# Kernel optimization log

Measured on AMD Instinct MI355X. Metric: run time of the kernel, lower is better.

Reference implementation:

```python
import jax, jax.numpy as jnp
import numpy as np

N_HEAD = 16

def setup_inputs() -> dict:
    key = jax.random.key(0)
    k1, k2, k3, k4, k5 = jax.random.split(key, 5)
    B, S, D = 2, 2048, 1024
    return {
        "hidden_states": jax.random.normal(k1, (B, S, D), jnp.float32),
        "w_attn": jax.random.normal(k2, (D, 3 * D), jnp.float32) * 0.02,
        "b_attn": jax.random.normal(k3, (3 * D,), jnp.float32) * 0.02,
        "w_proj": jax.random.normal(k4, (D, D), jnp.float32) * 0.02,
        "b_proj": jax.random.normal(k5, (D,), jnp.float32) * 0.02,
    }

def reference(hidden_states, w_attn, b_attn, w_proj, b_proj):
    B, S, D = hidden_states.shape
    H = N_HEAD
    Dh = D // H
    qkv = hidden_states @ w_attn + b_attn              # [B,S,3D]
    q, k, v = jnp.split(qkv, 3, axis=-1)
    def split_heads(x):
        return x.reshape(B, S, H, Dh).transpose(0, 2, 1, 3)  # [B,H,S,Dh]
    q, k, v = split_heads(q), split_heads(k), split_heads(v)
    # scale=True: divide by sqrt(head_dim) (v.size(-1))
    scores = jnp.einsum("bhqd,bhkd->bhqk", q, k) / jnp.sqrt(jnp.float32(Dh))
    attn = jax.nn.softmax(scores, axis=-1)             # [B,H,S,S]
    out = jnp.einsum("bhqk,bhkd->bhqd", attn, v)       # [B,H,S,Dh]
    out = out.transpose(0, 2, 1, 3).reshape(B, S, D)   # merge heads
    return out @ w_proj + b_proj
```

## Files before the change

kernel.cpp:

```cpp
#include <hip/hip_runtime.h>
#include <hip/hip_bf16.h>

typedef __attribute__((ext_vector_type(8))) short bf16x8;
typedef __attribute__((ext_vector_type(4))) float f32x4;
typedef __attribute__((ext_vector_type(16))) float f32x16;

#define LOG2E 1.4426950408889634f
#define SCALE_F (0.125f * LOG2E)

__device__ inline unsigned short f2bf(float f) {
  union { float f; unsigned u; } x; x.f = f;
  unsigned u = x.u;
  unsigned r = u + 0x7FFFu + ((u >> 16) & 1u);
  return (unsigned short)(r >> 16);
}

__device__ inline unsigned cvtpk(float lo, float hi) {
  unsigned r;
  asm("v_cvt_pk_bf16_f32 %0, %1, %2" : "=v"(r) : "v"(lo), "v"(hi));
  return r;
}

__device__ inline void gload16(const unsigned short* g, unsigned short* l) {
  __builtin_amdgcn_global_load_lds(
      (const __attribute__((address_space(1))) unsigned int*)g,
      (__attribute__((address_space(3))) unsigned int*)l, 16, 0, 0);
}

template <int J>
__device__ inline bf16x8 pack_pfrag(f32x16 p) {
  int X, Y, Z, W;
  asm("v_cvt_pk_bf16_f32 %0, %1, %2" : "=v"(X) : "v"(p[J + 0]), "v"(p[J + 1]));
  asm("v_cvt_pk_bf16_f32 %0, %1, %2" : "=v"(Y) : "v"(p[J + 2]), "v"(p[J + 3]));
  asm("v_cvt_pk_bf16_f32 %0, %1, %2" : "=v"(Z) : "v"(p[J + 4]), "v"(p[J + 5]));
  asm("v_cvt_pk_bf16_f32 %0, %1, %2" : "=v"(W) : "v"(p[J + 6]), "v"(p[J + 7]));
  asm("v_permlane32_swap_b32 %0, %1" : "+v"(X), "+v"(Z));
  asm("v_permlane32_swap_b32 %0, %1" : "+v"(Y), "+v"(W));
  union { int w[4]; bf16x8 v; } u;
  u.w[0] = X; u.w[1] = Y; u.w[2] = Z; u.w[3] = W;
  return u.v;
}

__device__ inline void transpose_tile(const float* __restrict__ W,
                                      unsigned short* __restrict__ WT, int K, int N,
                                      int n0, int k0, int t,
                                      unsigned short (*Tl)[72]) {
#pragma unroll
  for (int i = 0; i < 4; ++i) {
    int idx = t + i * 256;
    int r = idx >> 4, c4 = (idx & 15) << 2;
    float4 v = *reinterpret_cast<const float4*>(&W[(size_t)(k0 + r) * N + n0 + c4]);
    Tl[c4 + 0][r] = f2bf(v.x);
    Tl[c4 + 1][r] = f2bf(v.y);
    Tl[c4 + 2][r] = f2bf(v.z);
    Tl[c4 + 3][r] = f2bf(v.w);
  }
  __syncthreads();
#pragma unroll
  for (int i = 0; i < 2; ++i) {
    int idx = t + i * 256;
    int rr = idx >> 3, cc = (idx & 7) << 3;
    *reinterpret_cast<int4*>(&WT[(size_t)(n0 + rr) * K + k0 + cc]) =
        *reinterpret_cast<const int4*>(&Tl[rr][cc]);
  }
}

__global__ __launch_bounds__(256) void prep_fused(
    const float* __restrict__ hs, unsigned short* __restrict__ hs_b,
    const float* __restrict__ w_attn, unsigned short* __restrict__ wT,
    const float* __restrict__ w_proj, unsigned short* __restrict__ pT) {
  __shared__ unsigned short Tl[64][72];
  const int bid = blockIdx.x, t = threadIdx.x;
  if (bid < 768) {
    transpose_tile(w_attn, wT, 1024, 3072, (bid % 48) * 64, (bid / 48) * 64, t, Tl);
  } else if (bid < 1024) {
    int r = bid - 768;
    transpose_tile(w_proj, pT, 1024, 1024, (r % 16) * 64, (r / 16) * 64, t, Tl);
  } else {
    int cb = bid - 1024;
#pragma unroll
    for (int j = 0; j < 4; ++j) {
      int i = cb * 1024 + j * 256 + t;
      float4 v = reinterpret_cast<const float4*>(hs)[i];
      ushort4 o;
      o.x = f2bf(v.x); o.y = f2bf(v.y); o.z = f2bf(v.z); o.w = f2bf(v.w);
      reinterpret_cast<ushort4*>(hs_b)[i] = o;
    }
  }
}

__global__ __launch_bounds__(512, 2) void gemm_qkv_8p(
    const unsigned short* __restrict__ A, const unsigned short* __restrict__ Bt,
    const float* __restrict__ bias,
    unsigned short* __restrict__ qw, unsigned short* __restrict__ kw,
    unsigned short* __restrict__ vtg) {
  __shared__ unsigned short Abuf[2][16384];
  __shared__ unsigned short Bbuf[2][12288];
  const int t = threadIdx.x, lane = t & 63, wid = t >> 6;
  const int wm = wid >> 2, wn = wid & 3;
  const int orig = blockIdx.x;
  const int nid = (orig & 7) * 32 + (orig >> 3);
  const int mt = nid >> 4, nt = nid & 15;
  const int row0 = mt * 256, col0 = nt * 192;
  const int lr = lane & 15, kq = lane >> 4;
  const int srow_lo = lane >> 3;
  const int scg = (lane & 7) ^ srow_lo;
  const unsigned short* Ab = A + (size_t)row0 * 1024;
  const unsigned short* Bb = Bt + (size_t)col0 * 1024;
  f32x4 acc[8][3] = {};

#define SA8(bs, kt)                                                              \
  {                                                                              \
    const unsigned short* Ap = Ab + (kt) * 64;                                   \
    _Pragma("unroll") for (int i = 0; i < 4; ++i) {                              \
      int g = wid * 4 + i;                                                       \
      int rrel = g * 8 + srow_lo;                                                \
      gload16(&Ap[(size_t)rrel * 1024 + scg * 8], &Abuf[bs][g * 512]);           \
    }                                                                            \
  }
#define SB8(bs, kt)                                                              \
  {                                                                              \
    const unsigned short* Bp = Bb + (kt) * 64;                                   \
    _Pragma("unroll") for (int i = 0; i < 3; ++i) {                              \
      int g = wid * 3 + i;                                                       \
      int rrel = g * 8 + srow_lo;                                                \
      gload16(&Bp[(size_t)rrel * 1024 + scg * 8], &Bbuf[bs][g * 512]);           \
    }                                                                            \
  }
#define RDA(dst, mh)                                                             \
  _Pragma("unroll") for (int m = 0; m < 4; ++m)                                  \
  _Pragma("unroll") for (int ks = 0; ks < 2; ++ks) {                             \
    int row = wm * 128 + (mh) * 64 + m * 16 + lr;                                \
    dst[m][ks] = *reinterpret_cast<const bf16x8*>(                               \
        &Ac[row * 64 + (((ks * 4 + kq) ^ (row & 7)) << 3)]);                     \
  }
#define RDB2(dst)                                                                \
  _Pragma("unroll") for (int n = 0; n < 2; ++n)                                  \
  _Pragma("unroll") for (int ks = 0; ks < 2; ++ks) {                             \
    int row = wn * 48 + n * 16 + lr;                                             \
    dst[n][ks] = *reinterpret_cast<const bf16x8*>(                               \
        &Bc[row * 64 + (((ks * 4 + kq) ^ (row & 7)) << 3)]);                     \
  }
#define RDB1(dst)                                                                \
  _Pragma("unroll") for (int ks = 0; ks < 2; ++ks) {                             \
    int row = wn * 48 + 32 + lr;                                                 \
    dst[0][ks] = *reinterpret_cast<const bf16x8*>(                               \
        &Bc[row * 64 + (((ks * 4 + kq) ^ (row & 7)) << 3)]);                     \
  }
#define QMM2(mh, afv, bfv)                                                       \
  _Pragma("unroll") for (int m = 0; m < 4; ++m)                                  \
  _Pragma("unroll") for (int n = 0; n < 2; ++n)                                  \
  _Pragma("unroll") for (int ks = 0; ks < 2; ++ks)                               \
    acc[(mh) * 4 + m][n] = __builtin_amdgcn_mfma_f32_16x16x32_bf16(              \
        afv[m][ks], bfv[n][ks], acc[(mh) * 4 + m][n], 0, 0, 0);
#define QMM1(mh, afv, bfv)                                                       \
  _Pragma("unroll") for (int m = 0; m < 4; ++m)                                  \
  _Pragma("unroll") for (int ks = 0; ks < 2; ++ks)                               \
    acc[(mh) * 4 + m][2] = __builtin_amdgcn_mfma_f32_16x16x32_bf16(              \
        afv[m][ks], bfv[0][ks], acc[(mh) * 4 + m][2], 0, 0, 0);
#define BAR8 __builtin_amdgcn_s_barrier();

  SA8(0, 0) SB8(0, 0)
  asm volatile("s_waitcnt vmcnt(0)" ::: "memory");
  BAR8
  __builtin_amdgcn_sched_barrier(0);

  for (int kt = 0; kt < 16; ++kt) {
    const int buf = kt & 1;
    const unsigned short* Ac = Abuf[buf];
    const unsigned short* Bc = Bbuf[buf];
    bf16x8 af0[4][2], af1[4][2], bf0[2][2], bf1[1][2];
    RDA(af0, 0) RDB2(bf0)
    if (kt < 15) SA8(buf ^ 1, kt + 1)
    BAR8
    __builtin_amdgcn_s_setprio(1); QMM2(0, af0, bf0) __builtin_amdgcn_s_setprio(0);
    BAR8
    RDA(af1, 1)
    if (kt < 15) SB8(buf ^ 1, kt + 1)
    BAR8
    __builtin_amdgcn_s_setprio(1); QMM2(1, af1, bf0) __builtin_amdgcn_s_setprio(0);
    BAR8
    RDB1(bf1)
    BAR8
    __builtin_amdgcn_s_setprio(1); QMM1(0, af0, bf1) __builtin_amdgcn_s_setprio(0);
    BAR8
    if (kt < 15) { asm volatile("s_waitcnt vmcnt(0)" ::: "memory"); }
    BAR8
    __builtin_amdgcn_s_setprio(1); QMM1(1, af1, bf1) __builtin_amdgcn_s_setprio(0);
    BAR8
    __builtin_amdgcn_sched_barrier(0);
  }
#undef SA8
#undef SB8
#undef RDA
#undef RDB2
#undef RDB1
#undef QMM2
#undef QMM1
#undef BAR8

  const int rbase = (lane >> 4) * 4;
#pragma unroll
  for (int mm = 0; mm < 8; ++mm) {
#pragma unroll
    for (int nn = 0; nn < 3; ++nn) {
      int c = col0 + wn * 48 + nn * 16 + lr;
      int which = c >> 10;
      int d = c & 1023;
      int h = d >> 6, dh = d & 63;
      float bv = bias[c];
      int m0 = row0 + wm * 128 + mm * 16 + rbase;
      int b = m0 >> 11, s0 = m0 & 2047;
      if (which == 2) {
        int kt = s0 >> 6, key0 = s0 & 63;
        ushort4 pv;
        pv.x = f2bf(acc[mm][nn][0] + bv);
        pv.y = f2bf(acc[mm][nn][1] + bv);
        pv.z = f2bf(acc[mm][nn][2] + bv);
        pv.w = f2bf(acc[mm][nn][3] + bv);
        *reinterpret_cast<ushort4*>(
            &vtg[(((size_t)(b * 16 + h) * 32 + kt) * 64 + dh) * 64 + key0]) = pv;
      } else if (which == 1) {
#pragma unroll
        for (int r = 0; r < 4; ++r)
          kw[(((size_t)b * 16 + h) * 2048 + (s0 + r)) * 64 + dh] = f2bf(acc[mm][nn][r] + bv);
      } else {
#pragma unroll
        for (int r = 0; r < 4; ++r)
          qw[(((size_t)b * 16 + h) * 2048 + (s0 + r)) * 64 + dh] =
              f2bf((acc[mm][nn][r] + bv) * SCALE_F);
      }
    }
  }
}

#define GST(bs, kt)                                                             \
  {                                                                             \
    const unsigned short* Ap = Ab + (kt) * 32;                                  \
    const unsigned short* Bp = Bb + (kt) * 32;                                  \
    _Pragma("unroll") for (int i = 0; i < 2; ++i) {                             \
      int row = i * 64 + wid * 16 + s_r;                                        \
      gload16(&Ap[(size_t)row * 1024 + s_c], &Al[bs][i * 2048 + wid * 512]);    \
      gload16(&Bp[(size_t)row * 1024 + s_c], &Bl[bs][i * 2048 + wid * 512]);    \
    }                                                                           \
  }

#define GBODY(br)                                                               \
  {                                                                             \
    bf16x8 af[4], bfv[4];                                                       \
    _Pragma("unroll") for (int mm = 0; mm < 4; ++mm) {                          \
      int row = wr + mm * 16 + lr;                                              \
      af[mm] = *reinterpret_cast<const bf16x8*>(                                \
          &Al[br][row * 32 + ((kq ^ (lr & 3)) << 3)]);                          \
    }                                                                           \
    _Pragma("unroll") for (int nn = 0; nn < 4; ++nn) {                          \
      int row = wc + nn * 16 + lr;                                              \
      bfv[nn] = *reinterpret_cast<const bf16x8*>(                               \
          &Bl[br][row * 32 + ((kq ^ (lr & 3)) << 3)]);                          \
    }                                                                           \
    _Pragma("unroll") for (int mm = 0; mm < 4; ++mm)                            \
      _Pragma("unroll") for (int nn = 0; nn < 4; ++nn)                          \
        acc[mm][nn] =                                                           \
            __builtin_amdgcn_mfma_f32_16x16x32_bf16(af[mm], bfv[nn],            \
                                                    acc[mm][nn], 0, 0, 0);      \
  }

#define VMC4 asm volatile("s_waitcnt vmcnt(4)" ::: "memory");
#define VMC0 asm volatile("s_waitcnt vmcnt(0)" ::: "memory");
#define BAR __builtin_amdgcn_s_barrier();

__global__ __launch_bounds__(256) void gemm_proj_b(
    const unsigned short* __restrict__ A, const unsigned short* __restrict__ Bt,
    const float* __restrict__ bias, float* __restrict__ out) {
  const int N = 1024;
  __shared__ unsigned short Al[3][4096];
  __shared__ unsigned short Bl[3][4096];
  const int t = threadIdx.x, lane = t & 63, wid = t >> 6;
  const int wr = (wid >> 1) * 64, wc = (wid & 1) * 64;
  const int orig = blockIdx.x + 8 * blockIdx.y;
  const int nid = (orig & 7) * 32 + (orig >> 3);
  const int row0 = (nid >> 3) * 128, col0 = (nid & 7) * 128;
  const int lr = lane & 15, kq = lane >> 4;
  const int s_r = lane >> 2;
  const int s_c = ((lane & 3) ^ (s_r & 3)) * 8;
  const unsigned short* Ab = A + (size_t)row0 * 1024;
  const unsigned short* Bb = Bt + (size_t)col0 * 1024;
  f32x4 acc[4][4] = {};

  GST(0, 0) GST(1, 1)
  VMC4 BAR
  for (int tt = 0; tt < 30; tt += 3) {
    GST(2, tt + 2) GBODY(0) VMC4 BAR
    GST(0, tt + 3) GBODY(1) VMC4 BAR
    GST(1, tt + 4) GBODY(2) VMC4 BAR
  }
  GBODY(0) VMC0 BAR
  GBODY(1)

  const int rbase = (lane >> 4) * 4;
#pragma unroll
  for (int mm = 0; mm < 4; ++mm) {
#pragma unroll
    for (int nn = 0; nn < 4; ++nn) {
      int c = col0 + wc + nn * 16 + lr;
      float bv = bias[c];
#pragma unroll
      for (int r = 0; r < 4; ++r) {
        int m = row0 + wr + mm * 16 + rbase + r;
        out[(size_t)m * N + c] = acc[mm][nn][r] + bv;
      }
    }
  }
}

__global__ __launch_bounds__(512, 4) void attn_kernel(
    const unsigned short* __restrict__ qw, const unsigned short* __restrict__ kw,
    const unsigned short* __restrict__ vtg, unsigned short* __restrict__ ow) {
  __shared__ char smem[65536];
  unsigned short* KV = (unsigned short*)smem;
  unsigned short* Ol = (unsigned short*)smem;
  float* EX = (float*)(smem + 18432);
  const int t = threadIdx.x, lane = t & 63, wid = t >> 6;
  const int half = wid >> 2, wq = wid & 3;
  const int l31 = lane & 31, hi = lane >> 5;
  const int orig = blockIdx.x + 16 * blockIdx.y;
  const int nid = (orig & 7) * 64 + (orig >> 3);
  const int qt = nid & 15, bh = nid >> 4;
  const int b = bh >> 4, h = bh & 15;
  const unsigned short* Qg = qw + (size_t)bh * 2048 * 64;
  const unsigned short* Kg = kw + (size_t)bh * 2048 * 64;
  const unsigned short* Vg = vtg + (size_t)bh * 32 * 4096;
  const int q0 = qt * 128 + wq * 32;

  bf16x8 qf[4];
#pragma unroll
  for (int kc = 0; kc < 4; ++kc)
    qf[kc] = *reinterpret_cast<const bf16x8*>(&Qg[(q0 + l31) * 64 + kc * 16 + hi * 8]);

  f32x16 oA = {0,0,0,0,0,0,0,0,0,0,0,0,0,0,0,0};
  f32x16 oB = {0,0,0,0,0,0,0,0,0,0,0,0,0,0,0,0};
  float lrun = 0.f;

  const int srow_lo = lane >> 3;
  const int scg0 = (lane & 7) ^ srow_lo;
  const int rsw = (l31 & 7) ^ ((l31 >> 3) & 3);

#define STAGE(buf, kt)                                                              \
  {                                                                                 \
    const unsigned short* Kt = Kg + (size_t)(kt) * 4096;                            \
    const unsigned short* Vs = Vg + (size_t)(kt) * 4096;                            \
    unsigned short* Kl = KV + half * 16384 + (buf) * 8192;                          \
    unsigned short* Vl = Kl + 4096;                                                 \
    _Pragma("unroll") for (int i = 0; i < 2; ++i) {                                 \
      int chunk = wq * 2 + i;                                                       \
      int row = chunk * 8 + srow_lo;                                                \
      int sc = (scg0 ^ (chunk & 3)) * 8;                                            \
      gload16(&Kt[row * 64 + sc], &Kl[chunk * 512]);                                \
      gload16(&Vs[row * 64 + sc], &Vl[chunk * 512]);                                \
    }                                                                               \
  }

  const int kt0 = half * 16;
  STAGE(0, kt0)

  for (int it = 0; it < 16; ++it) {
    const int cur = it & 1;
    if (it + 1 < 16) {
      STAGE(cur ^ 1, kt0 + it + 1)
      asm volatile("s_waitcnt vmcnt(4)" ::: "memory");
    } else {
      asm volatile("s_waitcnt vmcnt(0)" ::: "memory");
    }
    __builtin_amdgcn_s_barrier();
    const unsigned short* Kl = KV + half * 16384 + cur * 8192;
    const unsigned short* Vl = Kl + 4096;

    f32x16 sA = {0,0,0,0,0,0,0,0,0,0,0,0,0,0,0,0};
    f32x16 sB = {0,0,0,0,0,0,0,0,0,0,0,0,0,0,0,0};
    __builtin_amdgcn_s_setprio(1);
#pragma unroll
    for (int kc = 0; kc < 4; ++kc) {
      bf16x8 k0f = *reinterpret_cast<const bf16x8*>(
          &Kl[l31 * 64 + (((kc * 2 + hi) ^ rsw) << 3)]);
      bf16x8 k1f = *reinterpret_cast<const bf16x8*>(
          &Kl[(32 + l31) * 64 + (((kc * 2 + hi) ^ rsw) << 3)]);
      sA = __builtin_amdgcn_mfma_f32_32x32x16_bf16(k0f, qf[kc], sA, 0, 0, 0);
      sB = __builtin_amdgcn_mfma_f32_32x32x16_bf16(k1f, qf[kc], sB, 0, 0, 0);
    }
    __builtin_amdgcn_s_setprio(0);

    float rsv[16];
#pragma unroll
    for (int j = 0; j < 16; ++j) {
      float pa = exp2f(sA[j]);
      float pb = exp2f(sB[j]);
      sA[j] = pa; sB[j] = pb;
      rsv[j] = pa + pb;
    }
#pragma unroll
    for (int s = 8; s >= 1; s >>= 1)
#pragma unroll
      for (int j = 0; j < s; ++j) rsv[j] += rsv[j + s];
    lrun += rsv[0] + __shfl_xor(rsv[0], 32);

    bf16x8 pf0 = pack_pfrag<0>(sA);
    bf16x8 pf1 = pack_pfrag<8>(sA);
    bf16x8 pf2 = pack_pfrag<0>(sB);
    bf16x8 pf3 = pack_pfrag<8>(sB);

    __builtin_amdgcn_s_setprio(1);
#pragma unroll
    for (int c = 0; c < 4; ++c) {
      bf16x8 pf = (c == 0) ? pf0 : (c == 1) ? pf1 : (c == 2) ? pf2 : pf3;
      int g = c * 2 + hi;
      bf16x8 v0f = *reinterpret_cast<const bf16x8*>(
          &Vl[l31 * 64 + ((g ^ rsw) << 3)]);
      bf16x8 v1f = *reinterpret_cast<const bf16x8*>(
          &Vl[(32 + l31) * 64 + ((g ^ rsw) << 3)]);
      oA = __builtin_amdgcn_mfma_f32_32x32x16_bf16(v0f, pf, oA, 0, 0, 0);
      oB = __builtin_amdgcn_mfma_f32_32x32x16_bf16(v1f, pf, oB, 0, 0, 0);
    }
    __builtin_amdgcn_s_setprio(0);
    __builtin_amdgcn_s_barrier();
  }
#undef STAGE

  __syncthreads();
  if (half == 1) {
    float* e = EX + ((size_t)(wq * 64 + lane)) * 34;
#pragma unroll
    for (int j = 0; j < 16; ++j) { e[j] = oA[j]; e[16 + j] = oB[j]; }
    e[32] = lrun;
  }
  __syncthreads();
  if (half == 0) {
    const float* e = EX + ((size_t)(wq * 64 + lane)) * 34;
    float linv = 1.0f / (lrun + e[32]);
    unsigned short* orow_l = Ol + (wq * 32 + l31) * 72;
#pragma unroll
    for (int g = 0; g < 4; ++g) {
      float a0 = (oA[4 * g + 0] + e[4 * g + 0]) * linv;
      float a1v = (oA[4 * g + 1] + e[4 * g + 1]) * linv;
      float a2v = (oA[4 * g + 2] + e[4 * g + 2]) * linv;
      float a3v = (oA[4 * g + 3] + e[4 * g + 3]) * linv;
      uint2 w0; w0.x = cvtpk(a0, a1v); w0.y = cvtpk(a2v, a3v);
      *reinterpret_cast<uint2*>(&orow_l[8 * g + 4 * hi]) = w0;
      float b0 = (oB[4 * g + 0] + e[16 + 4 * g + 0]) * linv;
      float b1v = (oB[4 * g + 1] + e[16 + 4 * g + 1]) * linv;
      float b2v = (oB[4 * g + 2] + e[16 + 4 * g + 2]) * linv;
      float b3v = (oB[4 * g + 3] + e[16 + 4 * g + 3]) * linv;
      uint2 w1; w1.x = cvtpk(b0, b1v); w1.y = cvtpk(b2v, b3v);
      *reinterpret_cast<uint2*>(&orow_l[32 + 8 * g + 4 * hi]) = w1;
    }
  }
  __syncthreads();
#pragma unroll
  for (int i = 0; i < 2; ++i) {
    int idx = t + i * 512;
    int q = idx >> 3, ch = idx & 7;
    int4 v = *reinterpret_cast<const int4*>(&Ol[q * 72 + ch * 8]);
    *reinterpret_cast<int4*>(
        &ow[(((size_t)b * 2048 + qt * 128 + q) * 16 + h) * 64 + ch * 8]) = v;
  }
}

extern "C" void kernel_launch(void* const* d_in, const int* in_sizes, int n_in,
                              void* d_out, int out_size, void* d_ws, size_t ws_size,
                              hipStream_t stream) {
  const float* hs = (const float*)d_in[0];
  const float* w_attn = (const float*)d_in[1];
  const float* b_attn = (const float*)d_in[2];
  const float* w_proj = (const float*)d_in[3];
  const float* b_proj = (const float*)d_in[4];
  float* out = (float*)d_out;

  const size_t HEAD = (size_t)2 * 16 * 2048 * 64;
  unsigned short* qw = (unsigned short*)d_ws;
  unsigned short* kw = qw + HEAD;
  unsigned short* vtg = kw + HEAD;
  unsigned short* hs_b = vtg + HEAD;
  unsigned short* ow = hs_b;
  unsigned short* wT = hs_b + HEAD;
  unsigned short* pT = wT + (size_t)3072 * 1024;

  prep_fused<<<dim3(2048), 256, 0, stream>>>(hs, hs_b, w_attn, wT, w_proj, pT);

  gemm_qkv_8p<<<dim3(256), 512, 0, stream>>>(hs_b, wT, b_attn, qw, kw, vtg);
  attn_kernel<<<dim3(16, 32), 512, 0, stream>>>(qw, kw, vtg, ow);
  gemm_proj_b<<<dim3(8, 32), 256, 0, stream>>>(ow, pT, b_proj, out);
}
```

Baseline: 118.9 us.

## Rewrite projection GEMM as 8-wave ping-pong kernel and reorder attention staging

Replaces the 4-wave triple-buffered projection GEMM with an 8-wave kernel. It uses 64-wide K tiles, double buffering and barrier-separated halves so that LDS reads, global prefetch and MFMA phases interleave across waves. In the attention loop, the prefetch of the next K/V tile now issues after the barrier that follows a full wait, and the trailing barrier is removed. This is meant to raise occupancy and overlap in the projection and cut one barrier per attention iteration. The trade-offs are extra barriers in the GEMM and a prefetch that no longer overlaps the wait in attention.

```diff
diff --git a/kernel.cpp b/kernel.cpp
--- a/kernel.cpp
+++ b/kernel.cpp
@@ -234,80 +234,95 @@
   }
 }
 
-#define GST(bs, kt)                                                             \
-  {                                                                             \
-    const unsigned short* Ap = Ab + (kt) * 32;                                  \
-    const unsigned short* Bp = Bb + (kt) * 32;                                  \
-    _Pragma("unroll") for (int i = 0; i < 2; ++i) {                             \
-      int row = i * 64 + wid * 16 + s_r;                                        \
-      gload16(&Ap[(size_t)row * 1024 + s_c], &Al[bs][i * 2048 + wid * 512]);    \
-      gload16(&Bp[(size_t)row * 1024 + s_c], &Bl[bs][i * 2048 + wid * 512]);    \
-    }                                                                           \
-  }
-
-#define GBODY(br)                                                               \
-  {                                                                             \
-    bf16x8 af[4], bfv[4];                                                       \
-    _Pragma("unroll") for (int mm = 0; mm < 4; ++mm) {                          \
-      int row = wr + mm * 16 + lr;                                              \
-      af[mm] = *reinterpret_cast<const bf16x8*>(                                \
-          &Al[br][row * 32 + ((kq ^ (lr & 3)) << 3)]);                          \
-    }                                                                           \
-    _Pragma("unroll") for (int nn = 0; nn < 4; ++nn) {                          \
-      int row = wc + nn * 16 + lr;                                              \
-      bfv[nn] = *reinterpret_cast<const bf16x8*>(                               \
-          &Bl[br][row * 32 + ((kq ^ (lr & 3)) << 3)]);                          \
-    }                                                                           \
-    _Pragma("unroll") for (int mm = 0; mm < 4; ++mm)                            \
-      _Pragma("unroll") for (int nn = 0; nn < 4; ++nn)                          \
-        acc[mm][nn] =                                                           \
-            __builtin_amdgcn_mfma_f32_16x16x32_bf16(af[mm], bfv[nn],            \
-                                                    acc[mm][nn], 0, 0, 0);      \
-  }
-
-#define VMC4 asm volatile("s_waitcnt vmcnt(4)" ::: "memory");
-#define VMC0 asm volatile("s_waitcnt vmcnt(0)" ::: "memory");
-#define BAR __builtin_amdgcn_s_barrier();
-
-__global__ __launch_bounds__(256) void gemm_proj_b(
+__global__ __launch_bounds__(512, 4) void gemm_proj_8p(
     const unsigned short* __restrict__ A, const unsigned short* __restrict__ Bt,
     const float* __restrict__ bias, float* __restrict__ out) {
-  const int N = 1024;
-  __shared__ unsigned short Al[3][4096];
-  __shared__ unsigned short Bl[3][4096];
+  __shared__ unsigned short Abuf[2][8192];
+  __shared__ unsigned short Bbuf[2][8192];
   const int t = threadIdx.x, lane = t & 63, wid = t >> 6;
-  const int wr = (wid >> 1) * 64, wc = (wid & 1) * 64;
-  const int orig = blockIdx.x + 8 * blockIdx.y;
+  const int wm = wid >> 2, wn = wid & 3;
+  const int orig = blockIdx.x;
   const int nid = (orig & 7) * 32 + (orig >> 3);
   const int row0 = (nid >> 3) * 128, col0 = (nid & 7) * 128;
   const int lr = lane & 15, kq = lane >> 4;
-  const int s_r = lane >> 2;
-  const int s_c = ((lane & 3) ^ (s_r & 3)) * 8;
+  const int srow_lo = lane >> 3;
+  const int scg = (lane & 7) ^ srow_lo;
   const unsigned short* Ab = A + (size_t)row0 * 1024;
   const unsigned short* Bb = Bt + (size_t)col0 * 1024;
-  f32x4 acc[4][4] = {};
-
-  GST(0, 0) GST(1, 1)
-  VMC4 BAR
-  for (int tt = 0; tt < 30; tt += 3) {
-    GST(2, tt + 2) GBODY(0) VMC4 BAR
-    GST(0, tt + 3) GBODY(1) VMC4 BAR
-    GST(1, tt + 4) GBODY(2) VMC4 BAR
-  }
-  GBODY(0) VMC0 BAR
-  GBODY(1)
+  f32x4 acc[4][2] = {};
+
+#define SP(bs, kt)                                                               \
+  {                                                                              \
+    const unsigned short* Ap = Ab + (kt) * 64;                                   \
+    const unsigned short* Bp = Bb + (kt) * 64;                                   \
+    _Pragma("unroll") for (int i = 0; i < 2; ++i) {                              \
+      int g = wid * 2 + i;                                                       \
+      int rrel = g * 8 + srow_lo;                                                \
+      gload16(&Ap[(size_t)rrel * 1024 + scg * 8], &Abuf[bs][g * 512]);           \
+      gload16(&Bp[(size_t)rrel * 1024 + scg * 8], &Bbuf[bs][g * 512]);           \
+    }                                                                            \
+  }
+#define RPA(dst, mh)                                                             \
+  _Pragma("unroll") for (int m = 0; m < 2; ++m)                                  \
+  _Pragma("unroll") for (int ks = 0; ks < 2; ++ks) {                             \
+    int row = wm * 64 + (mh) * 32 + m * 16 + lr;                                 \
+    dst[m][ks] = *reinterpret_cast<const bf16x8*>(                               \
+        &Ac[row * 64 + (((ks * 4 + kq) ^ (row & 7)) << 3)]);                     \
+  }
+#define RPB(dst)                                                                 \
+  _Pragma("unroll") for (int n = 0; n < 2; ++n)                                  \
+  _Pragma("unroll") for (int ks = 0; ks < 2; ++ks) {                             \
+    int row = wn * 32 + n * 16 + lr;                                             \
+    dst[n][ks] = *reinterpret_cast<const bf16x8*>(                               \
+        &Bc[row * 64 + (((ks * 4 + kq) ^ (row & 7)) << 3)]);                     \
+  }
+#define PMM(mh, afv, bfv)                                                        \
+  _Pragma("unroll") for (int m = 0; m < 2; ++m)                                  \
+  _Pragma("unroll") for (int n = 0; n < 2; ++n)                                  \
+  _Pragma("unroll") for (int ks = 0; ks < 2; ++ks)                               \
+    acc[(mh) * 2 + m][n] = __builtin_amdgcn_mfma_f32_16x16x32_bf16(              \
+        afv[m][ks], bfv[n][ks], acc[(mh) * 2 + m][n], 0, 0, 0);
+#define BARP __builtin_amdgcn_s_barrier();
+
+  SP(0, 0)
+  asm volatile("s_waitcnt vmcnt(0)" ::: "memory");
+  BARP
+  __builtin_amdgcn_sched_barrier(0);
+
+  for (int kt = 0; kt < 16; ++kt) {
+    const int buf = kt & 1;
+    const unsigned short* Ac = Abuf[buf];
+    const unsigned short* Bc = Bbuf[buf];
+    bf16x8 af0[2][2], af1[2][2], bfv[2][2];
+    RPA(af0, 0) RPB(bfv)
+    if (kt < 15) SP(buf ^ 1, kt + 1)
+    BARP
+    __builtin_amdgcn_s_setprio(1); PMM(0, af0, bfv) __builtin_amdgcn_s_setprio(0);
+    BARP
+    RPA(af1, 1)
+    if (kt < 15) { asm volatile("s_waitcnt vmcnt(0)" ::: "memory"); }
+    BARP
+    __builtin_amdgcn_s_setprio(1); PMM(1, af1, bfv) __builtin_amdgcn_s_setprio(0);
+    BARP
+    __builtin_amdgcn_sched_barrier(0);
+  }
+#undef SP
+#undef RPA
+#undef RPB
+#undef PMM
+#undef BARP
 
   const int rbase = (lane >> 4) * 4;
 #pragma unroll
   for (int mm = 0; mm < 4; ++mm) {
 #pragma unroll
-    for (int nn = 0; nn < 4; ++nn) {
-      int c = col0 + wc + nn * 16 + lr;
+    for (int nn = 0; nn < 2; ++nn) {
+      int c = col0 + wn * 32 + nn * 16 + lr;
       float bv = bias[c];
 #pragma unroll
       for (int r = 0; r < 4; ++r) {
-        int m = row0 + wr + mm * 16 + rbase + r;
-        out[(size_t)m * N + c] = acc[mm][nn][r] + bv;
+        int m = row0 + wm * 64 + mm * 16 + rbase + r;
+        out[(size_t)m * 1024 + c] = acc[mm][nn][r] + bv;
       }
     }
   }
@@ -365,13 +380,9 @@
 
   for (int it = 0; it < 16; ++it) {
     const int cur = it & 1;
-    if (it + 1 < 16) {
-      STAGE(cur ^ 1, kt0 + it + 1)
-      asm volatile("s_waitcnt vmcnt(4)" ::: "memory");
-    } else {
-      asm volatile("s_waitcnt vmcnt(0)" ::: "memory");
-    }
+    asm volatile("s_waitcnt vmcnt(0)" ::: "memory");
     __builtin_amdgcn_s_barrier();
+    if (it + 1 < 16) STAGE(cur ^ 1, kt0 + it + 1)
     const unsigned short* Kl = KV + half * 16384 + cur * 8192;
     const unsigned short* Vl = Kl + 4096;
 
@@ -421,7 +432,6 @@
       oB = __builtin_amdgcn_mfma_f32_32x32x16_bf16(v1f, pf, oB, 0, 0, 0);
     }
     __builtin_amdgcn_s_setprio(0);
-    __builtin_amdgcn_s_barrier();
   }
 #undef STAGE
 
@@ -487,5 +497,5 @@
 
   gemm_qkv_8p<<<dim3(256), 512, 0, stream>>>(hs_b, wT, b_attn, qw, kw, vtg);
   attn_kernel<<<dim3(16, 32), 512, 0, stream>>>(qw, kw, vtg, ow);
-  gemm_proj_b<<<dim3(8, 32), 256, 0, stream>>>(ow, pT, b_proj, out);
-}
+  gemm_proj_8p<<<dim3(256), 512, 0, stream>>>(ow, pT, b_proj, out);
+}
```

Result: faster. 115.3 us (-3.0%).
